# Kernel optimization log

Measured on AMD Instinct MI355X. Metric: run time of the kernel, lower is better.

## Reference

```python
import jax, jax.numpy as jnp
import numpy as np

N_TH1 = 33
N_TH2 = 2 * (N_TH1 - 1) + 1
LB, UB = 1e-20, 1e20
LB_EXP, UB_EXP = -20.0, 20.0


def _make_directions():
    # Spherical direction grid, matching the TF constructor loop order.
    th1 = np.linspace(-np.pi / 2, np.pi / 2, N_TH1)
    th2 = np.linspace(-np.pi, np.pi, N_TH2)
    c1, s1 = np.cos(th1), np.sin(th1)
    c2, s2 = np.cos(th2), np.sin(th2)
    i = np.arange(1, N_TH1 - 1)
    j = np.arange(N_TH2 - 1)
    dx = np.outer(c1[i], c2[j]).ravel()
    dy = np.outer(c1[i], s2[j]).ravel()
    dz = np.repeat(s1[i], len(j))
    d = np.stack([dx, dy, dz], axis=-1)
    poles = np.array([[c1[0] * c2[0], c1[0] * s2[0], s1[0]],
                      [c1[-1] * c2[0], c1[-1] * s2[0], s1[-1]]])
    return jnp.asarray(np.concatenate([d, poles], 0), jnp.float32)  # [D,3]


def _spt(dirs, local_v, smoothness, trans):
    # dirs [D,3], local_v [B,P,V,3], smoothness [B,P], trans [B,P,1,3]
    z = jnp.einsum('bpvc,dc->bpvd', local_v, dirs)            # [B,P,V,D]
    zm = jnp.where(z > 0, z, 0.0)
    p = smoothness[:, :, None, None]                          # [B,P,1,1]
    # Overflow-safe exponent scaling: pick k=10^ceil(lk) so max(zm*k)^p >= 1e-20.
    zm_log = jnp.log10(jnp.max(zm, axis=2, keepdims=True))    # [B,P,1,D]
    exponent = zm_log * p
    lk = jnp.where(exponent < LB_EXP, (LB_EXP - exponent) / p, 0.0)
    k = jnp.power(10.0, jnp.clip(jnp.ceil(lk), 0.0, UB_EXP))  # [B,P,1,D]
    k = jax.lax.stop_gradient(k)  # ceil has zero grad in the original too
    zms = zm * k
    pos = zms > 0
    # clip(zm^p, LB, UB) - (zm==0)*LB  ==  where(zm>0, clip(zm^p,LB,UB), 0)
    zm_p = jnp.where(pos, jnp.clip(jnp.where(pos, zms, 1.0) ** p, LB, UB), 0.0)
    sum_zm_p = jnp.sum(zm_p, axis=2, keepdims=True)           # [B,P,1,D]
    h = jnp.clip(sum_zm_p ** (1.0 / p), LB, UB)               # [B,P,1,D]
    ratio = jnp.where(pos, zms, 1.0) / h
    dhdz = jnp.where(pos, jnp.clip(ratio ** (p - 1.0), LB, UB), LB)  # [B,P,V,D]
    surf = jnp.einsum('bpvd,bpvc->bpdc', dhdz, local_v) + trans      # [B,P,D,3]
    h_out = jnp.transpose(jnp.clip(h / k, -UB, UB), (0, 1, 3, 2))    # [B,P,D,1]
    return h_out, surf


def setup_inputs() -> dict:
    key = jax.random.key(0)
    k1, k2 = jax.random.split(key)
    vertices = jax.random.normal(k1, (8, 16, 64, 3), dtype=jnp.float32)
    # smoothness p in [2, 20] (positive power-norm exponent)
    smoothness = 2.0 + 18.0 * jax.random.uniform(k2, (8, 16), dtype=jnp.float32)
    return {'vertices': vertices, 'smoothness': smoothness}


def reference(vertices, smoothness):
    dirs = _make_directions()                                 # [D,3]
    mean_v = jnp.mean(vertices, axis=2, keepdims=True)        # [B,P,1,3]
    local_v = vertices - mean_v
    h, surf = _spt(dirs, local_v, smoothness, mean_v)
    B, P = vertices.shape[0], vertices.shape[1]
    D = dirs.shape[0]
    local_dirs = jnp.broadcast_to(dirs, (B, P, D, 3))
    direction_h = jnp.concatenate([local_dirs, h], axis=-1)   # [B,P,D,4]
    points = surf.reshape(B, P * D, 3)                        # [B, P*D, 3]
    overlap = jnp.zeros((B, P, 1), jnp.float32)               # overlap routine truncated in source
    mean_out = mean_v.reshape(B, P, 3)
    return (points, direction_h, overlap, mean_out, dirs, local_v)
```

## Files before the change

### kernel.cpp

```cpp
#include <hip/hip_runtime.h>

#define NB 8
#define NP 16
#define NV 64
#define ND 1986

#define OFF_POINTS 0
#define OFF_DH     762624
#define OFF_OVER   1779456
#define OFF_MEAN   1779584
#define OFF_DIRS   1779968
#define OFF_LOCALV 1785926

__global__ __launch_bounds__(256, 4) void mcx_kernel(
    const float* __restrict__ verts,
    const float* __restrict__ smooth,
    float* __restrict__ out)
{
    const int t     = threadIdx.x;
    const int bp    = blockIdx.x >> 4;
    const int chunk = blockIdx.x & 15;
    const int dl    = t >> 1;
    const int half  = t & 1;
    const int d     = chunk * 128 + dl;

    __shared__ float lv[NV][4];
    __shared__ float mean_sh[3];

    const int v3 = t / 3;
    const int c3 = t - v3 * 3;
    if (t < 192) lv[v3][c3] = verts[bp * 192 + t];
    else         lv[t - 192][3] = 0.f;
    __syncthreads();
    if (t < 3) {
        float s = 0.f;
        for (int v = 0; v < NV; ++v) s += lv[v][t];
        mean_sh[t] = s * (1.f / 64.f);
    }
    __syncthreads();
    const float m0 = mean_sh[0], m1 = mean_sh[1], m2 = mean_sh[2];
    if (t < 192) lv[v3][c3] -= mean_sh[c3];
    __syncthreads();

    if (chunk == 0) {
        if (t < 192) out[OFF_LOCALV + bp * 192 + t] = lv[v3][c3];
        if (t < 3)   out[OFF_MEAN + bp * 3 + t] = mean_sh[t];
        if (t == 3)  out[OFF_OVER + bp] = 0.f;
    }

    if (d >= ND) return;

    int i, j;
    if (d < 1984) { i = 1 + (d >> 6); j = d & 63; }
    else          { i = (d == 1984) ? 0 : 32; j = 0; }
    const double STEP = 3.141592653589793 / 32.0;
    const float th1 = (float)(-1.5707963267948966 + (double)i * STEP);
    const float th2 = (float)(-3.141592653589793  + (double)j * STEP);
    const float c1 = cosf(th1), s1 = sinf(th1);
    const float c2 = cosf(th2), s2 = sinf(th2);
    const float dx = c1 * c2, dy = c1 * s2, dz = s1;
    if (bp == 0 && half == 0) {
        out[OFF_DIRS + d * 3 + 0] = dx;
        out[OFF_DIRS + d * 3 + 1] = dy;
        out[OFF_DIRS + d * 3 + 2] = dz;
    }

    const float sm  = smooth[bp];
    const float ip  = 1.0f / sm;
    const float pm1 = sm - 1.0f;
    const int voff  = half * 32;

    float zv[32];
    float m = 0.f;
    #pragma unroll
    for (int v = 0; v < 32; ++v) {
        const float* q = lv[voff + v];
        float z = fmaf(q[0], dx, fmaf(q[1], dy, q[2] * dz));
        z = fmaxf(z, 0.f);
        zv[v] = z;
        m = fmaxf(m, z);
    }
    m = fmaxf(m, __shfl_xor(m, 1, 64));
    m = fmaxf(m, 1e-37f);
    const float lm = __log2f(m);

    float sum = 0.f;
    #pragma unroll
    for (int v = 0; v < 32; ++v) {
        float lz = __log2f(zv[v]) - lm;
        zv[v] = lz;
        sum += exp2f(sm * lz);
    }
    sum += __shfl_xor(sum, 1, 64);
    const float lh = ip * __log2f(fmaxf(sum, 1e-30f));

    float sx = 0.f, sy = 0.f, sz = 0.f;
    #pragma unroll
    for (int v = 0; v < 32; ++v) {
        float dh = exp2f(pm1 * (zv[v] - lh));
        const float* q = lv[voff + v];
        sx = fmaf(dh, q[0], sx);
        sy = fmaf(dh, q[1], sy);
        sz = fmaf(dh, q[2], sz);
    }
    sx += __shfl_xor(sx, 1, 64);
    sy += __shfl_xor(sy, 1, 64);
    sz += __shfl_xor(sz, 1, 64);

    const float hout = m * exp2f(lh);

    const int idx = bp * ND + d;
    if (half == 0) {
        out[OFF_POINTS + idx * 3 + 0] = sx + m0;
        out[OFF_POINTS + idx * 3 + 1] = sy + m1;
        out[OFF_POINTS + idx * 3 + 2] = sz + m2;
    } else {
        out[OFF_DH + idx * 4 + 0] = dx;
        out[OFF_DH + idx * 4 + 1] = dy;
        out[OFF_DH + idx * 4 + 2] = dz;
        out[OFF_DH + idx * 4 + 3] = hout;
    }
}

extern "C" void kernel_launch(void* const* d_in, const int* in_sizes, int n_in,
                              void* d_out, int out_size, void* d_ws, size_t ws_size,
                              hipStream_t stream) {
    const float* verts  = (const float*)d_in[0];
    const float* smooth = (const float*)d_in[1];
    float* out = (float*)d_out;
    (void)d_ws; (void)ws_size; (void)in_sizes; (void)n_in; (void)out_size;
    mcx_kernel<<<dim3(NB * NP * 16), dim3(256), 0, stream>>>(verts, smooth, out);
}
```

Measured before the change: 72.62 us.

## Split vertices across 4 lanes, cache them in registers, loop directions per block

Each direction is now handled by four lanes with 16 vertices each instead of two lanes with 32. Each lane keeps its vertex slice in registers and reuses it across four direction groups. Grid size is halved, so the per-block setup (loading vertices, computing the mean) is amortised over more directions. It also swaps in raw hardware exp2/log2 and fast sin/cos, folds constants into FMAs, writes direction_h as one float4 store, and spreads output stores over more lanes. Fast intrinsics and dropping the sum clamp may change accuracy slightly, and fewer blocks lowers parallelism.

After: 71.27 us. No clear change (-1.9%).

```diff
diff --git a/kernel.cpp b/kernel.cpp
--- a/kernel.cpp
+++ b/kernel.cpp
@@ -12,113 +12,122 @@
 #define OFF_DIRS   1779968
 #define OFF_LOCALV 1785926
 
+__device__ __forceinline__ float fexp2(float x) { return __builtin_amdgcn_exp2f(x); }
+__device__ __forceinline__ float flog2(float x) { return __builtin_amdgcn_logf(x); }
+
 __global__ __launch_bounds__(256, 4) void mcx_kernel(
     const float* __restrict__ verts,
     const float* __restrict__ smooth,
     float* __restrict__ out)
 {
     const int t     = threadIdx.x;
-    const int bp    = blockIdx.x >> 4;
-    const int chunk = blockIdx.x & 15;
-    const int dl    = t >> 1;
-    const int half  = t & 1;
-    const int d     = chunk * 128 + dl;
+    const int bp    = blockIdx.x >> 3;
+    const int chunk = blockIdx.x & 7;
+    const int quad  = t >> 2;
+    const int lane4 = t & 3;
 
-    __shared__ float lv[NV][4];
-    __shared__ float mean_sh[3];
+    __shared__ float4 lv4[NV];
+    __shared__ float  mean_sh[3];
+    float* lvf = (float*)lv4;
 
     const int v3 = t / 3;
     const int c3 = t - v3 * 3;
-    if (t < 192) lv[v3][c3] = verts[bp * 192 + t];
-    else         lv[t - 192][3] = 0.f;
+    if (t < 192) lvf[v3 * 4 + c3] = verts[bp * 192 + t];
+    else if (t < 256) lvf[(t - 192) * 4 + 3] = 0.f;
     __syncthreads();
     if (t < 3) {
         float s = 0.f;
-        for (int v = 0; v < NV; ++v) s += lv[v][t];
+        for (int v = 0; v < NV; ++v) s += lvf[v * 4 + t];
         mean_sh[t] = s * (1.f / 64.f);
     }
     __syncthreads();
     const float m0 = mean_sh[0], m1 = mean_sh[1], m2 = mean_sh[2];
-    if (t < 192) lv[v3][c3] -= mean_sh[c3];
+    if (t < 192) lvf[v3 * 4 + c3] -= mean_sh[c3];
     __syncthreads();
 
     if (chunk == 0) {
-        if (t < 192) out[OFF_LOCALV + bp * 192 + t] = lv[v3][c3];
+        if (t < 192) out[OFF_LOCALV + bp * 192 + t] = lvf[v3 * 4 + c3];
         if (t < 3)   out[OFF_MEAN + bp * 3 + t] = mean_sh[t];
         if (t == 3)  out[OFF_OVER + bp] = 0.f;
     }
 
-    if (d >= ND) return;
-
-    int i, j;
-    if (d < 1984) { i = 1 + (d >> 6); j = d & 63; }
-    else          { i = (d == 1984) ? 0 : 32; j = 0; }
-    const double STEP = 3.141592653589793 / 32.0;
-    const float th1 = (float)(-1.5707963267948966 + (double)i * STEP);
-    const float th2 = (float)(-3.141592653589793  + (double)j * STEP);
-    const float c1 = cosf(th1), s1 = sinf(th1);
-    const float c2 = cosf(th2), s2 = sinf(th2);
-    const float dx = c1 * c2, dy = c1 * s2, dz = s1;
-    if (bp == 0 && half == 0) {
-        out[OFF_DIRS + d * 3 + 0] = dx;
-        out[OFF_DIRS + d * 3 + 1] = dy;
-        out[OFF_DIRS + d * 3 + 2] = dz;
+    float vxr[16], vyr[16], vzr[16];
+    #pragma unroll
+    for (int k = 0; k < 16; ++k) {
+        float4 q = lv4[lane4 * 16 + k];
+        vxr[k] = q.x; vyr[k] = q.y; vzr[k] = q.z;
     }
 
     const float sm  = smooth[bp];
-    const float ip  = 1.0f / sm;
-    const float pm1 = sm - 1.0f;
-    const int voff  = half * 32;
+    const float ip  = 1.f / sm;
+    const float pm1 = sm - 1.f;
 
-    float zv[32];
-    float m = 0.f;
-    #pragma unroll
-    for (int v = 0; v < 32; ++v) {
-        const float* q = lv[voff + v];
-        float z = fmaf(q[0], dx, fmaf(q[1], dy, q[2] * dz));
-        z = fmaxf(z, 0.f);
-        zv[v] = z;
-        m = fmaxf(m, z);
-    }
-    m = fmaxf(m, __shfl_xor(m, 1, 64));
-    m = fmaxf(m, 1e-37f);
-    const float lm = __log2f(m);
+    #pragma unroll 1
+    for (int g = 0; g < 4; ++g) {
+        const int d = chunk * 256 + g * 64 + quad;
+        if (d >= ND) continue;
 
-    float sum = 0.f;
-    #pragma unroll
-    for (int v = 0; v < 32; ++v) {
-        float lz = __log2f(zv[v]) - lm;
-        zv[v] = lz;
-        sum += exp2f(sm * lz);
-    }
-    sum += __shfl_xor(sum, 1, 64);
-    const float lh = ip * __log2f(fmaxf(sum, 1e-30f));
+        int i, j;
+        if (d < 1984) { i = 1 + (d >> 6); j = d & 63; }
+        else          { i = (d == 1984) ? 0 : 32; j = 0; }
+        const float th1 = (float)(-1.5707963267948966 + (double)i * 0.09817477042468103);
+        const float th2 = (float)(-3.141592653589793  + (double)j * 0.09817477042468103);
+        const float c1 = __cosf(th1), s1 = __sinf(th1);
+        const float c2 = __cosf(th2), s2 = __sinf(th2);
+        const float dx = c1 * c2, dy = c1 * s2, dz = s1;
 
-    float sx = 0.f, sy = 0.f, sz = 0.f;
-    #pragma unroll
-    for (int v = 0; v < 32; ++v) {
-        float dh = exp2f(pm1 * (zv[v] - lh));
-        const float* q = lv[voff + v];
-        sx = fmaf(dh, q[0], sx);
-        sy = fmaf(dh, q[1], sy);
-        sz = fmaf(dh, q[2], sz);
-    }
-    sx += __shfl_xor(sx, 1, 64);
-    sy += __shfl_xor(sy, 1, 64);
-    sz += __shfl_xor(sz, 1, 64);
+        float zv[16];
+        float m = 0.f;
+        #pragma unroll
+        for (int k = 0; k < 16; ++k) {
+            float z = fmaf(vxr[k], dx, fmaf(vyr[k], dy, vzr[k] * dz));
+            z = fmaxf(z, 0.f);
+            zv[k] = z;
+            m = fmaxf(m, z);
+        }
+        m = fmaxf(m, __shfl_xor(m, 1, 64));
+        m = fmaxf(m, __shfl_xor(m, 2, 64));
+        m = fmaxf(m, 1e-37f);
+        const float lm = flog2(m);
 
-    const float hout = m * exp2f(lh);
+        const float nslm = -sm * lm;
+        float sum = 0.f;
+        #pragma unroll
+        for (int k = 0; k < 16; ++k) {
+            float l = flog2(zv[k]);
+            zv[k] = l;
+            sum += fexp2(fmaf(sm, l, nslm));
+        }
+        sum += __shfl_xor(sum, 1, 64);
+        sum += __shfl_xor(sum, 2, 64);
+        const float lh = ip * flog2(sum);
 
-    const int idx = bp * ND + d;
-    if (half == 0) {
-        out[OFF_POINTS + idx * 3 + 0] = sx + m0;
-        out[OFF_POINTS + idx * 3 + 1] = sy + m1;
-        out[OFF_POINTS + idx * 3 + 2] = sz + m2;
-    } else {
-        out[OFF_DH + idx * 4 + 0] = dx;
-        out[OFF_DH + idx * 4 + 1] = dy;
-        out[OFF_DH + idx * 4 + 2] = dz;
-        out[OFF_DH + idx * 4 + 3] = hout;
+        const float cc = -pm1 * (lm + lh);
+        float sx = 0.f, sy = 0.f, sz = 0.f;
+        #pragma unroll
+        for (int k = 0; k < 16; ++k) {
+            float dh = fexp2(fmaf(pm1, zv[k], cc));
+            sx = fmaf(dh, vxr[k], sx);
+            sy = fmaf(dh, vyr[k], sy);
+            sz = fmaf(dh, vzr[k], sz);
+        }
+        sx += __shfl_xor(sx, 1, 64); sx += __shfl_xor(sx, 2, 64);
+        sy += __shfl_xor(sy, 1, 64); sy += __shfl_xor(sy, 2, 64);
+        sz += __shfl_xor(sz, 1, 64); sz += __shfl_xor(sz, 2, 64);
+
+        const int idx = bp * ND + d;
+        if (lane4 == 0) {
+            out[OFF_POINTS + idx * 3 + 0] = sx + m0;
+            out[OFF_POINTS + idx * 3 + 1] = sy + m1;
+            out[OFF_POINTS + idx * 3 + 2] = sz + m2;
+        } else if (lane4 == 1) {
+            const float hout = m * fexp2(lh);
+            ((float4*)out)[(OFF_DH >> 2) + idx] = make_float4(dx, dy, dz, hout);
+        } else if (lane4 == 2 && bp == 0) {
+            out[OFF_DIRS + d * 3 + 0] = dx;
+            out[OFF_DIRS + d * 3 + 1] = dy;
+            out[OFF_DIRS + d * 3 + 2] = dz;
+        }
     }
 }
 
@@ -129,5 +138,5 @@
     const float* smooth = (const float*)d_in[1];
     float* out = (float*)d_out;
     (void)d_ws; (void)ws_size; (void)in_sizes; (void)n_in; (void)out_size;
-    mcx_kernel<<<dim3(NB * NP * 16), dim3(256), 0, stream>>>(verts, smooth, out);
+    mcx_kernel<<<dim3(NB * NP * 8), dim3(256), 0, stream>>>(verts, smooth, out);
 }
```
